# Kernel optimization log

Measured on AMD Instinct MI355X. Metric: run time of the kernel, lower is better.

The kernel has to match this reference:

```python
import jax, jax.numpy as jnp
import numpy as np

H = 2048      # hidden_size
L = 350       # max_length

def setup_inputs() -> dict:
    key = jax.random.key(0)
    ks = jax.random.split(key, 12)
    s = 0.02
    return {
        "input": jax.random.normal(ks[0], (1, 1, H), jnp.float32),
        "hidden": jax.random.normal(ks[1], (1, 1, H), jnp.float32),
        "encoder_outputs": jax.random.normal(ks[2], (L, H), jnp.float32),
        # nn.Linear(2H, L)
        "attn_W": jax.random.normal(ks[3], (L, 2 * H), jnp.float32) * s,
        "attn_b": jax.random.normal(ks[4], (L,), jnp.float32) * s,
        # nn.Linear(2H, H)
        "comb_W": jax.random.normal(ks[5], (H, 2 * H), jnp.float32) * s,
        "comb_b": jax.random.normal(ks[6], (H,), jnp.float32) * s,
        # nn.GRU(H, H) single layer weights (PyTorch layout: [3H, H])
        "w_ih": jax.random.normal(ks[7], (3 * H, H), jnp.float32) * s,
        "w_hh": jax.random.normal(ks[8], (3 * H, H), jnp.float32) * s,
        "b_ih": jax.random.normal(ks[9], (3 * H,), jnp.float32) * s,
        "b_hh": jax.random.normal(ks[10], (3 * H,), jnp.float32) * s,
    }

def reference(input, hidden, encoder_outputs, attn_W, attn_b, comb_W, comb_b, w_ih, w_hh, b_ih, b_hh):
    x = input.reshape(1, H)          # (1, H)  == reshape(input,(1,1,H))[0]
    h = hidden[0]                    # (1, H)
    # Bahdanau-style attention over fixed max_length slots
    attn_weights = jax.nn.softmax(jnp.concatenate([x, h], axis=1) @ attn_W.T + attn_b, axis=1)  # (1, L)
    context = attn_weights @ encoder_outputs                                                    # (1, H)
    # combine + relu (dropout is defined but never applied in the original forward)
    g = jax.nn.relu(jnp.concatenate([x, context], axis=1) @ comb_W.T + comb_b)                  # (1, H)
    # single GRU step (PyTorch gate order: reset, update, new)
    gi = g @ w_ih.T + b_ih           # (1, 3H)
    gh = h @ w_hh.T + b_hh           # (1, 3H)
    i_r, i_z, i_n = jnp.split(gi, 3, axis=1)
    h_r, h_z, h_n = jnp.split(gh, 3, axis=1)
    r = jax.nn.sigmoid(i_r + h_r)
    z = jax.nn.sigmoid(i_z + h_z)
    n = jnp.tanh(i_n + r * h_n)
    h_new = (1.0 - z) * n + z * h    # (1, H)
    output = h_new[None]             # (1, 1, H)
    return (output, h_new[None], attn_weights)
```

## Files before the change

### kernel.cpp

```cpp
#include <hip/hip_runtime.h>
#include <math.h>

#define H 2048
#define L 350
#define NB 1024
#define NREP 16
#define MAGIC 0x7FC0FFEEu
#define BOUND 65536

#define LOG_B0 0
#define CTX_B0 88
#define GHB_B0 152

#define OFF_GH   512
#define OFF_CTXR 8192
#define OFF_GR   40960
#define OFF_MK   73728

#define SLOTA 0
#define SLOTB (88*16)
#define SLOTC (SLOTB+64*16)
#define SLOTG (SLOTC+912*16)
#define SUPC  (SLOTG+1024*16)
#define SUPG  (SUPC+32*16)

#define VMCNT0() asm volatile("s_waitcnt vmcnt(0)" ::: "memory")

__device__ __forceinline__ float cload(const float* p) {
    return __hip_atomic_load(p, __ATOMIC_RELAXED, __HIP_MEMORY_SCOPE_AGENT);
}
__device__ __forceinline__ void cstore(float* p, float v) {
    __hip_atomic_store(p, v, __ATOMIC_RELAXED, __HIP_MEMORY_SCOPE_AGENT);
}
__device__ __forceinline__ unsigned long long cload64(const unsigned long long* p) {
    return __hip_atomic_load(p, __ATOMIC_RELAXED, __HIP_MEMORY_SCOPE_AGENT);
}
__device__ __forceinline__ void postmk(unsigned* p) {
    __hip_atomic_store(p, MAGIC, __ATOMIC_RELAXED, __HIP_MEMORY_SCOPE_SYSTEM);
}
__device__ __forceinline__ unsigned peekmk(const unsigned* p) {
    return __hip_atomic_load(p, __ATOMIC_RELAXED, __HIP_MEMORY_SCOPE_SYSTEM);
}
__device__ __forceinline__ void waitslots(const unsigned* base, int n) {
    const int t = threadIdx.x;
    for (int s = t; s < n; s += 256)
        for (int it = 0; it < BOUND; ++it) {
            if (peekmk(&base[s * 16]) == MAGIC) break;
            __builtin_amdgcn_s_sleep(8);
        }
    __syncthreads();
}

__device__ __forceinline__ float dot4(float4 a, float4 b, float acc) {
    acc = fmaf(a.x, b.x, acc);
    acc = fmaf(a.y, b.y, acc);
    acc = fmaf(a.z, b.z, acc);
    acc = fmaf(a.w, b.w, acc);
    return acc;
}
__device__ __forceinline__ float wsum(float v) {
    #pragma unroll
    for (int m = 1; m < 64; m <<= 1) v += __shfl_xor(v, m, 64);
    return v;
}
__device__ __forceinline__ float wmax(float v) {
    #pragma unroll
    for (int m = 1; m < 64; m <<= 1) v = fmaxf(v, __shfl_xor(v, m, 64));
    return v;
}

__device__ __forceinline__ void gh_row(int row, int lane,
    const float4* h4, const float* w_hh, const float* b_hh, float* gh)
{
    const float4* Wr = reinterpret_cast<const float4*>(w_hh + (size_t)row * H);
    float a0 = 0.f, a1 = 0.f, a2 = 0.f, a3 = 0.f;
    #pragma unroll
    for (int k = 0; k < 8; k += 4) {
        a0 = dot4(Wr[lane + (k + 0) * 64], h4[lane + (k + 0) * 64], a0);
        a1 = dot4(Wr[lane + (k + 1) * 64], h4[lane + (k + 1) * 64], a1);
        a2 = dot4(Wr[lane + (k + 2) * 64], h4[lane + (k + 2) * 64], a2);
        a3 = dot4(Wr[lane + (k + 3) * 64], h4[lane + (k + 3) * 64], a3);
    }
    const float acc = wsum((a0 + a1) + (a2 + a3));
    if (lane == 0) cstore(&gh[row], acc + b_hh[row]);
}

__global__ __launch_bounds__(256, 4) void fused_decoder(
    const float* __restrict__ input, const float* __restrict__ hidden,
    const float* __restrict__ enc,
    const float* __restrict__ attn_W, const float* __restrict__ attn_b,
    const float* __restrict__ comb_W, const float* __restrict__ comb_b,
    const float* __restrict__ w_ih, const float* __restrict__ w_hh,
    const float* __restrict__ b_ih, const float* __restrict__ b_hh,
    float* __restrict__ out, float* __restrict__ ws)
{
    __shared__ __align__(16) float sh[2048];
    __shared__ float smax[4], ssum[4];
    __shared__ float part[8][32];
    __shared__ float red[4];
    __shared__ float p3[4][3];

    float* logits = ws;
    float* gh     = ws + OFF_GH;
    float* ctxrep = ws + OFF_CTXR;
    float* grep   = ws + OFF_GR;
    unsigned* mk  = (unsigned*)(ws + OFF_MK);

    const int b = blockIdx.x, tid = threadIdx.x;
    const int wv = tid >> 6, lane = tid & 63;
    const float4* x4 = reinterpret_cast<const float4*>(input);
    const float4* h4 = reinterpret_cast<const float4*>(hidden);

    if (b < CTX_B0) {
        const int r = b * 4 + wv;
        if (r < L) {
            const float4* Wr = reinterpret_cast<const float4*>(attn_W + (size_t)r * (2 * H));
            float a0 = 0.f, a1 = 0.f, a2 = 0.f, a3 = 0.f;
            #pragma unroll
            for (int k = 0; k < 8; k += 4) {
                a0 = dot4(Wr[lane + (k+0)*64], x4[lane + (k+0)*64], a0);
                a1 = dot4(Wr[lane + (k+1)*64], x4[lane + (k+1)*64], a1);
                a2 = dot4(Wr[lane + (k+2)*64], x4[lane + (k+2)*64], a2);
                a3 = dot4(Wr[lane + (k+3)*64], x4[lane + (k+3)*64], a3);
            }
            #pragma unroll
            for (int k = 0; k < 8; k += 4) {
                a0 = dot4(Wr[512 + lane + (k+0)*64], h4[lane + (k+0)*64], a0);
                a1 = dot4(Wr[512 + lane + (k+1)*64], h4[lane + (k+1)*64], a1);
                a2 = dot4(Wr[512 + lane + (k+2)*64], h4[lane + (k+2)*64], a2);
                a3 = dot4(Wr[512 + lane + (k+3)*64], h4[lane + (k+3)*64], a3);
            }
            const float acc = wsum((a0 + a1) + (a2 + a3));
            if (lane == 0) cstore(&logits[r], acc + attn_b[r]);
        }
        VMCNT0();
        __syncthreads();
        if (tid == 0) postmk(&mk[SLOTA + b * 16]);
        if (b < 40) {
            if (wv == 0) gh_row(6104 + b, lane, h4, w_hh, b_hh, gh);
            VMCNT0();
            __syncthreads();
            if (tid == 0) postmk(&mk[SLOTC + (872 + b) * 16]);
        }
    } else if (b < GHB_B0) {
        const int cb = b - CTX_B0;
        waitslots(&mk[SLOTA], 88);
        float v0 = (tid < L) ? cload(&logits[tid]) : -INFINITY;
        float v1 = (tid + 256 < L) ? cload(&logits[tid + 256]) : -INFINITY;
        float m = wmax(fmaxf(v0, v1));
        if (lane == 0) smax[wv] = m;
        __syncthreads();
        m = fmaxf(fmaxf(smax[0], smax[1]), fmaxf(smax[2], smax[3]));
        float e0 = (tid < L) ? expf(v0 - m) : 0.f;
        float e1 = (tid + 256 < L) ? expf(v1 - m) : 0.f;
        float s = wsum(e0 + e1);
        if (lane == 0) ssum[wv] = s;
        __syncthreads();
        const float inv = 1.f / (ssum[0] + ssum[1] + ssum[2] + ssum[3]);
        if (tid < L) sh[tid] = e0 * inv;
        if (tid + 256 < L) sh[tid + 256] = e1 * inv;
        if (cb == 0) {
            if (tid < L) out[2 * H + tid] = e0 * inv;
            if (tid + 256 < L) out[2 * H + tid + 256] = e1 * inv;
        }
        __syncthreads();
        const int col_l = tid & 31, k = tid >> 5;
        const float* ec = enc + cb * 32 + col_l;
        float a0 = 0.f, a1 = 0.f, a2 = 0.f, a3 = 0.f;
        int j = k;
        for (; j + 24 < L; j += 32) {
            a0 = fmaf(sh[j],      ec[(size_t)j * H],        a0);
            a1 = fmaf(sh[j + 8],  ec[(size_t)(j + 8) * H],  a1);
            a2 = fmaf(sh[j + 16], ec[(size_t)(j + 16) * H], a2);
            a3 = fmaf(sh[j + 24], ec[(size_t)(j + 24) * H], a3);
        }
        for (; j < L; j += 8) a0 = fmaf(sh[j], ec[(size_t)j * H], a0);
        part[k][col_l] = (a0 + a1) + (a2 + a3);
        __syncthreads();
        if (tid < 32) {
            const float acc = part[0][tid] + part[1][tid] + part[2][tid] + part[3][tid]
                            + part[4][tid] + part[5][tid] + part[6][tid] + part[7][tid];
            #pragma unroll
            for (int rp = 0; rp < NREP; ++rp)
                cstore(&ctxrep[rp * 2048 + cb * 32 + tid], acc);
        }
        VMCNT0();
        __syncthreads();
        if (tid == 0) postmk(&mk[SLOTB + cb * 16]);
    } else {
        const int m = b - GHB_B0;
        #pragma unroll
        for (int j = 0; j < 7; ++j)
            if ((j & 3) == wv) gh_row(m * 7 + j, lane, h4, w_hh, b_hh, gh);
        VMCNT0();
        __syncthreads();
        if (tid == 0) postmk(&mk[SLOTC + m * 16]);
    }

    waitslots(&mk[SLOTB], 64);
    {
        unsigned long long* sh64 = reinterpret_cast<unsigned long long*>(sh);
        const unsigned long long* c64 =
            reinterpret_cast<const unsigned long long*>(ctxrep + (b & (NREP - 1)) * 2048);
        for (int i = tid; i < H / 2; i += 256) sh64[i] = cload64(&c64[i]);
    }
    __syncthreads();
    {
        const float4* c4 = reinterpret_cast<const float4*>(sh);
        #pragma unroll
        for (int rr = 0; rr < 2; ++rr) {
            const int r = b * 2 + rr;
            const float4* Wr = reinterpret_cast<const float4*>(comb_W + (size_t)r * (2 * H));
            float a0 = dot4(Wr[tid],       x4[tid],       0.f);
            float a1 = dot4(Wr[tid + 256], x4[tid + 256], 0.f);
            float a2 = dot4(Wr[tid + 512], c4[tid],       0.f);
            float a3 = dot4(Wr[tid + 768], c4[tid + 256], 0.f);
            const float acc = wsum((a0 + a1) + (a2 + a3));
            if (lane == 0) red[wv] = acc;
            __syncthreads();
            if (tid == 0) {
                const float gval = fmaxf(red[0] + red[1] + red[2] + red[3] + comb_b[r], 0.f);
                #pragma unroll
                for (int rp = 0; rp < NREP; ++rp) cstore(&grep[rp * 2048 + r], gval);
            }
            __syncthreads();
        }
    }
    VMCNT0();
    if (tid == 0) postmk(&mk[SLOTG + b * 16]);

    if (b >= 88 && b < 120) {
        const int w = b - 88;
        const int cfrom = w * 29, cto = (cfrom + 29 < 912) ? cfrom + 29 : 912;
        if (tid < cto - cfrom) {
            for (int it = 0; it < BOUND; ++it) {
                if (peekmk(&mk[SLOTC + (cfrom + tid) * 16]) == MAGIC) break;
                __builtin_amdgcn_s_sleep(8);
            }
        } else if (tid >= 64 && tid < 96) {
            for (int it = 0; it < BOUND; ++it) {
                if (peekmk(&mk[SLOTG + (w * 32 + tid - 64) * 16]) == MAGIC) break;
                __builtin_amdgcn_s_sleep(8);
            }
        }
        __syncthreads();
        if (tid == 0) { postmk(&mk[SUPC + w * 16]); postmk(&mk[SUPG + w * 16]); }
    }

    {
        const int t = tid;
        if (t < 32) {
            for (int it = 0; it < BOUND; ++it) {
                if (peekmk(&mk[SUPC + t * 16]) == MAGIC) break;
                __builtin_amdgcn_s_sleep(8);
            }
        } else if (t >= 64 && t < 96) {
            for (int it = 0; it < BOUND; ++it) {
                if (peekmk(&mk[SUPG + (t - 64) * 16]) == MAGIC) break;
                __builtin_amdgcn_s_sleep(8);
            }
        }
        __syncthreads();
    }
    {
        unsigned long long* sh64 = reinterpret_cast<unsigned long long*>(sh);
        const unsigned long long* g64 =
            reinterpret_cast<const unsigned long long*>(grep + (b & (NREP - 1)) * 2048);
        for (int i = tid; i < H / 2; i += 256) sh64[i] = cload64(&g64[i]);
    }
    __syncthreads();
    {
        const float4* g4 = reinterpret_cast<const float4*>(sh);
        #pragma unroll
        for (int cc = 0; cc < 2; ++cc) {
            const int col = b * 2 + cc;
            const float4* W0 = reinterpret_cast<const float4*>(w_ih + (size_t)col * H);
            const float4* W1 = reinterpret_cast<const float4*>(w_ih + (size_t)(col + H) * H);
            const float4* W2 = reinterpret_cast<const float4*>(w_ih + (size_t)(col + 2 * H) * H);
            const float4 gv0 = g4[tid], gv1 = g4[tid + 256];
            float ar = dot4(W0[tid], gv0, 0.f); ar = dot4(W0[tid + 256], gv1, ar);
            float az = dot4(W1[tid], gv0, 0.f); az = dot4(W1[tid + 256], gv1, az);
            float an = dot4(W2[tid], gv0, 0.f); an = dot4(W2[tid + 256], gv1, an);
            ar = wsum(ar); az = wsum(az); an = wsum(an);
            if (lane == 0) { p3[wv][0] = ar; p3[wv][1] = az; p3[wv][2] = an; }
            __syncthreads();
            if (tid == 0) {
                const float ir  = p3[0][0] + p3[1][0] + p3[2][0] + p3[3][0] + b_ih[col];
                const float iz  = p3[0][1] + p3[1][1] + p3[2][1] + p3[3][1] + b_ih[col + H];
                const float in_ = p3[0][2] + p3[1][2] + p3[2][2] + p3[3][2] + b_ih[col + 2 * H];
                const float r = 1.f / (1.f + expf(-(ir + cload(&gh[col]))));
                const float z = 1.f / (1.f + expf(-(iz + cload(&gh[col + H]))));
                const float n = tanhf(in_ + r * cload(&gh[col + 2 * H]));
                const float hnew = (1.f - z) * n + z * hidden[col];
                out[col] = hnew;
                out[H + col] = hnew;
            }
            __syncthreads();
        }
    }
}

extern "C" void kernel_launch(void* const* d_in, const int* in_sizes, int n_in,
                              void* d_out, int out_size, void* d_ws, size_t ws_size,
                              hipStream_t stream)
{
    const float* input  = (const float*)d_in[0];
    const float* hidden = (const float*)d_in[1];
    const float* enc    = (const float*)d_in[2];
    const float* attn_W = (const float*)d_in[3];
    const float* attn_b = (const float*)d_in[4];
    const float* comb_W = (const float*)d_in[5];
    const float* comb_b = (const float*)d_in[6];
    const float* w_ih   = (const float*)d_in[7];
    const float* w_hh   = (const float*)d_in[8];
    const float* b_ih   = (const float*)d_in[9];
    const float* b_hh   = (const float*)d_in[10];
    float* out = (float*)d_out;
    float* ws  = (float*)d_ws;

    fused_decoder<<<NB, 256, 0, stream>>>(
        input, hidden, enc, attn_W, attn_b, comb_W, comb_b,
        w_ih, w_hh, b_ih, b_hh, out, ws);
}
```

Before: 32.17 us.

## Double block size to 512 threads and split rows across two thread teams

Blocks grow from 256 to 512 threads. Per-block work that used to run as two sequential iterations (two comb rows, two GRU columns) now runs as two 256-thread teams in parallel, which removes a loop and its barriers. The w_hh rows are rebalanced so the attention blocks' spare waves compute gh tail rows alongside the logits, and the gh blocks take 7 or 6 rows each. The aim is shorter per-block critical paths across the grid-wide flag chain. The risk is lower occupancy per CU with the larger blocks under launch_bounds(512,8), and every block must still be co-resident for the spin-wait barriers to work.

```diff
diff --git a/kernel.cpp b/kernel.cpp
--- a/kernel.cpp
+++ b/kernel.cpp
@@ -8,9 +8,9 @@
 #define MAGIC 0x7FC0FFEEu
 #define BOUND 65536
 
-#define LOG_B0 0
 #define CTX_B0 88
 #define GHB_B0 152
+#define GH_TAIL 5792
 
 #define OFF_GH   512
 #define OFF_CTXR 8192
@@ -20,7 +20,7 @@
 #define SLOTA 0
 #define SLOTB (88*16)
 #define SLOTC (SLOTB+64*16)
-#define SLOTG (SLOTC+912*16)
+#define SLOTG (SLOTC+960*16)
 #define SUPC  (SLOTG+1024*16)
 #define SUPG  (SUPC+32*16)
 
@@ -41,13 +41,14 @@
 __device__ __forceinline__ unsigned peekmk(const unsigned* p) {
     return __hip_atomic_load(p, __ATOMIC_RELAXED, __HIP_MEMORY_SCOPE_SYSTEM);
 }
+__device__ __forceinline__ void pollone(const unsigned* p) {
+    for (int it = 0; it < BOUND; ++it) {
+        if (peekmk(p) == MAGIC) break;
+        __builtin_amdgcn_s_sleep(8);
+    }
+}
 __device__ __forceinline__ void waitslots(const unsigned* base, int n) {
-    const int t = threadIdx.x;
-    for (int s = t; s < n; s += 256)
-        for (int it = 0; it < BOUND; ++it) {
-            if (peekmk(&base[s * 16]) == MAGIC) break;
-            __builtin_amdgcn_s_sleep(8);
-        }
+    for (int s = threadIdx.x; s < n; s += 512) pollone(&base[s * 16]);
     __syncthreads();
 }
 
@@ -85,7 +86,7 @@
     if (lane == 0) cstore(&gh[row], acc + b_hh[row]);
 }
 
-__global__ __launch_bounds__(256, 4) void fused_decoder(
+__global__ __launch_bounds__(512, 8) void fused_decoder(
     const float* __restrict__ input, const float* __restrict__ hidden,
     const float* __restrict__ enc,
     const float* __restrict__ attn_W, const float* __restrict__ attn_b,
@@ -95,10 +96,10 @@
     float* __restrict__ out, float* __restrict__ ws)
 {
     __shared__ __align__(16) float sh[2048];
-    __shared__ float smax[4], ssum[4];
-    __shared__ float part[8][32];
-    __shared__ float red[4];
-    __shared__ float p3[4][3];
+    __shared__ float smax[8], ssum[8];
+    __shared__ float part[16][32];
+    __shared__ float red[2][4];
+    __shared__ float p3[2][4][3];
 
     float* logits = ws;
     float* gh     = ws + OFF_GH;
@@ -112,74 +113,67 @@
     const float4* h4 = reinterpret_cast<const float4*>(hidden);
 
     if (b < CTX_B0) {
-        const int r = b * 4 + wv;
-        if (r < L) {
-            const float4* Wr = reinterpret_cast<const float4*>(attn_W + (size_t)r * (2 * H));
-            float a0 = 0.f, a1 = 0.f, a2 = 0.f, a3 = 0.f;
-            #pragma unroll
-            for (int k = 0; k < 8; k += 4) {
-                a0 = dot4(Wr[lane + (k+0)*64], x4[lane + (k+0)*64], a0);
-                a1 = dot4(Wr[lane + (k+1)*64], x4[lane + (k+1)*64], a1);
-                a2 = dot4(Wr[lane + (k+2)*64], x4[lane + (k+2)*64], a2);
-                a3 = dot4(Wr[lane + (k+3)*64], x4[lane + (k+3)*64], a3);
+        if (wv < 4) {
+            const int r = b * 4 + wv;
+            if (r < L) {
+                const float4* Wr = reinterpret_cast<const float4*>(attn_W + (size_t)r * (2 * H));
+                float a0 = 0.f, a1 = 0.f, a2 = 0.f, a3 = 0.f;
+                #pragma unroll
+                for (int k = 0; k < 8; k += 4) {
+                    a0 = dot4(Wr[lane + (k+0)*64], x4[lane + (k+0)*64], a0);
+                    a1 = dot4(Wr[lane + (k+1)*64], x4[lane + (k+1)*64], a1);
+                    a2 = dot4(Wr[lane + (k+2)*64], x4[lane + (k+2)*64], a2);
+                    a3 = dot4(Wr[lane + (k+3)*64], x4[lane + (k+3)*64], a3);
+                }
+                #pragma unroll
+                for (int k = 0; k < 8; k += 4) {
+                    a0 = dot4(Wr[512 + lane + (k+0)*64], h4[lane + (k+0)*64], a0);
+                    a1 = dot4(Wr[512 + lane + (k+1)*64], h4[lane + (k+1)*64], a1);
+                    a2 = dot4(Wr[512 + lane + (k+2)*64], h4[lane + (k+2)*64], a2);
+                    a3 = dot4(Wr[512 + lane + (k+3)*64], h4[lane + (k+3)*64], a3);
+                }
+                const float acc = wsum((a0 + a1) + (a2 + a3));
+                if (lane == 0) cstore(&logits[r], acc + attn_b[r]);
             }
-            #pragma unroll
-            for (int k = 0; k < 8; k += 4) {
-                a0 = dot4(Wr[512 + lane + (k+0)*64], h4[lane + (k+0)*64], a0);
-                a1 = dot4(Wr[512 + lane + (k+1)*64], h4[lane + (k+1)*64], a1);
-                a2 = dot4(Wr[512 + lane + (k+2)*64], h4[lane + (k+2)*64], a2);
-                a3 = dot4(Wr[512 + lane + (k+3)*64], h4[lane + (k+3)*64], a3);
-            }
-            const float acc = wsum((a0 + a1) + (a2 + a3));
-            if (lane == 0) cstore(&logits[r], acc + attn_b[r]);
+        } else {
+            gh_row(GH_TAIL + b * 4 + (wv - 4), lane, h4, w_hh, b_hh, gh);
         }
         VMCNT0();
         __syncthreads();
-        if (tid == 0) postmk(&mk[SLOTA + b * 16]);
-        if (b < 40) {
-            if (wv == 0) gh_row(6104 + b, lane, h4, w_hh, b_hh, gh);
-            VMCNT0();
-            __syncthreads();
-            if (tid == 0) postmk(&mk[SLOTC + (872 + b) * 16]);
-        }
+        if (tid == 0) { postmk(&mk[SLOTA + b * 16]); postmk(&mk[SLOTC + (872 + b) * 16]); }
     } else if (b < GHB_B0) {
         const int cb = b - CTX_B0;
         waitslots(&mk[SLOTA], 88);
         float v0 = (tid < L) ? cload(&logits[tid]) : -INFINITY;
-        float v1 = (tid + 256 < L) ? cload(&logits[tid + 256]) : -INFINITY;
-        float m = wmax(fmaxf(v0, v1));
+        float m = wmax(v0);
         if (lane == 0) smax[wv] = m;
         __syncthreads();
-        m = fmaxf(fmaxf(smax[0], smax[1]), fmaxf(smax[2], smax[3]));
+        m = fmaxf(fmaxf(fmaxf(smax[0], smax[1]), fmaxf(smax[2], smax[3])),
+                  fmaxf(fmaxf(smax[4], smax[5]), fmaxf(smax[6], smax[7])));
         float e0 = (tid < L) ? expf(v0 - m) : 0.f;
-        float e1 = (tid + 256 < L) ? expf(v1 - m) : 0.f;
-        float s = wsum(e0 + e1);
+        float s = wsum(e0);
         if (lane == 0) ssum[wv] = s;
         __syncthreads();
-        const float inv = 1.f / (ssum[0] + ssum[1] + ssum[2] + ssum[3]);
+        const float inv = 1.f / (((ssum[0] + ssum[1]) + (ssum[2] + ssum[3]))
+                               + ((ssum[4] + ssum[5]) + (ssum[6] + ssum[7])));
         if (tid < L) sh[tid] = e0 * inv;
-        if (tid + 256 < L) sh[tid + 256] = e1 * inv;
-        if (cb == 0) {
-            if (tid < L) out[2 * H + tid] = e0 * inv;
-            if (tid + 256 < L) out[2 * H + tid + 256] = e1 * inv;
-        }
+        if (cb == 0 && tid < L) out[2 * H + tid] = e0 * inv;
         __syncthreads();
         const int col_l = tid & 31, k = tid >> 5;
         const float* ec = enc + cb * 32 + col_l;
-        float a0 = 0.f, a1 = 0.f, a2 = 0.f, a3 = 0.f;
+        float a0 = 0.f, a1 = 0.f;
         int j = k;
-        for (; j + 24 < L; j += 32) {
+        for (; j + 16 < L; j += 32) {
             a0 = fmaf(sh[j],      ec[(size_t)j * H],        a0);
-            a1 = fmaf(sh[j + 8],  ec[(size_t)(j + 8) * H],  a1);
-            a2 = fmaf(sh[j + 16], ec[(size_t)(j + 16) * H], a2);
-            a3 = fmaf(sh[j + 24], ec[(size_t)(j + 24) * H], a3);
-        }
-        for (; j < L; j += 8) a0 = fmaf(sh[j], ec[(size_t)j * H], a0);
-        part[k][col_l] = (a0 + a1) + (a2 + a3);
+            a1 = fmaf(sh[j + 16], ec[(size_t)(j + 16) * H], a1);
+        }
+        for (; j < L; j += 16) a0 = fmaf(sh[j], ec[(size_t)j * H], a0);
+        part[k][col_l] = a0 + a1;
         __syncthreads();
         if (tid < 32) {
-            const float acc = part[0][tid] + part[1][tid] + part[2][tid] + part[3][tid]
-                            + part[4][tid] + part[5][tid] + part[6][tid] + part[7][tid];
+            float acc = 0.f;
+            #pragma unroll
+            for (int kk = 0; kk < 16; ++kk) acc += part[kk][tid];
             #pragma unroll
             for (int rp = 0; rp < NREP; ++rp)
                 cstore(&ctxrep[rp * 2048 + cb * 32 + tid], acc);
@@ -189,9 +183,9 @@
         if (tid == 0) postmk(&mk[SLOTB + cb * 16]);
     } else {
         const int m = b - GHB_B0;
-        #pragma unroll
-        for (int j = 0; j < 7; ++j)
-            if ((j & 3) == wv) gh_row(m * 7 + j, lane, h4, w_hh, b_hh, gh);
+        const int start = (m < 560) ? m * 7 : 3920 + (m - 560) * 6;
+        const int count = (m < 560) ? 7 : 6;
+        if (wv < count) gh_row(start + wv, lane, h4, w_hh, b_hh, gh);
         VMCNT0();
         __syncthreads();
         if (tid == 0) postmk(&mk[SLOTC + m * 16]);
@@ -202,100 +196,74 @@
         unsigned long long* sh64 = reinterpret_cast<unsigned long long*>(sh);
         const unsigned long long* c64 =
             reinterpret_cast<const unsigned long long*>(ctxrep + (b & (NREP - 1)) * 2048);
-        for (int i = tid; i < H / 2; i += 256) sh64[i] = cload64(&c64[i]);
-    }
-    __syncthreads();
-    {
+        for (int i = tid; i < H / 2; i += 512) sh64[i] = cload64(&c64[i]);
+    }
+    __syncthreads();
+    {
+        const int team = tid >> 8, ttid = tid & 255, twv = (tid >> 6) & 3;
         const float4* c4 = reinterpret_cast<const float4*>(sh);
-        #pragma unroll
-        for (int rr = 0; rr < 2; ++rr) {
-            const int r = b * 2 + rr;
-            const float4* Wr = reinterpret_cast<const float4*>(comb_W + (size_t)r * (2 * H));
-            float a0 = dot4(Wr[tid],       x4[tid],       0.f);
-            float a1 = dot4(Wr[tid + 256], x4[tid + 256], 0.f);
-            float a2 = dot4(Wr[tid + 512], c4[tid],       0.f);
-            float a3 = dot4(Wr[tid + 768], c4[tid + 256], 0.f);
-            const float acc = wsum((a0 + a1) + (a2 + a3));
-            if (lane == 0) red[wv] = acc;
-            __syncthreads();
-            if (tid == 0) {
-                const float gval = fmaxf(red[0] + red[1] + red[2] + red[3] + comb_b[r], 0.f);
-                #pragma unroll
-                for (int rp = 0; rp < NREP; ++rp) cstore(&grep[rp * 2048 + r], gval);
-            }
-            __syncthreads();
-        }
+        const int r = b * 2 + team;
+        const float4* Wr = reinterpret_cast<const float4*>(comb_W + (size_t)r * (2 * H));
+        float a0 = dot4(Wr[ttid],       x4[ttid],       0.f);
+        float a1 = dot4(Wr[ttid + 256], x4[ttid + 256], 0.f);
+        float a2 = dot4(Wr[ttid + 512], c4[ttid],       0.f);
+        float a3 = dot4(Wr[ttid + 768], c4[ttid + 256], 0.f);
+        const float acc = wsum((a0 + a1) + (a2 + a3));
+        if (lane == 0) red[team][twv] = acc;
+        __syncthreads();
+        if (ttid == 0) {
+            const float gval = fmaxf(red[team][0] + red[team][1] + red[team][2]
+                                     + red[team][3] + comb_b[r], 0.f);
+            #pragma unroll
+            for (int rp = 0; rp < NREP; ++rp) cstore(&grep[rp * 2048 + r], gval);
+        }
+        __syncthreads();
     }
     VMCNT0();
     if (tid == 0) postmk(&mk[SLOTG + b * 16]);
 
-    if (b >= 88 && b < 120) {
-        const int w = b - 88;
-        const int cfrom = w * 29, cto = (cfrom + 29 < 912) ? cfrom + 29 : 912;
-        if (tid < cto - cfrom) {
-            for (int it = 0; it < BOUND; ++it) {
-                if (peekmk(&mk[SLOTC + (cfrom + tid) * 16]) == MAGIC) break;
-                __builtin_amdgcn_s_sleep(8);
-            }
-        } else if (tid >= 64 && tid < 96) {
-            for (int it = 0; it < BOUND; ++it) {
-                if (peekmk(&mk[SLOTG + (w * 32 + tid - 64) * 16]) == MAGIC) break;
-                __builtin_amdgcn_s_sleep(8);
-            }
-        }
+    if (b >= CTX_B0 && b < CTX_B0 + 32) {
+        const int w = b - CTX_B0;
+        if (tid < 30) pollone(&mk[SLOTC + (w * 30 + tid) * 16]);
+        else if (tid >= 64 && tid < 96) pollone(&mk[SLOTG + (w * 32 + tid - 64) * 16]);
         __syncthreads();
         if (tid == 0) { postmk(&mk[SUPC + w * 16]); postmk(&mk[SUPG + w * 16]); }
     }
 
-    {
-        const int t = tid;
-        if (t < 32) {
-            for (int it = 0; it < BOUND; ++it) {
-                if (peekmk(&mk[SUPC + t * 16]) == MAGIC) break;
-                __builtin_amdgcn_s_sleep(8);
-            }
-        } else if (t >= 64 && t < 96) {
-            for (int it = 0; it < BOUND; ++it) {
-                if (peekmk(&mk[SUPG + (t - 64) * 16]) == MAGIC) break;
-                __builtin_amdgcn_s_sleep(8);
-            }
-        }
-        __syncthreads();
-    }
+    if (tid < 32) pollone(&mk[SUPC + tid * 16]);
+    else if (tid >= 64 && tid < 96) pollone(&mk[SUPG + (tid - 64) * 16]);
+    __syncthreads();
     {
         unsigned long long* sh64 = reinterpret_cast<unsigned long long*>(sh);
         const unsigned long long* g64 =
             reinterpret_cast<const unsigned long long*>(grep + (b & (NREP - 1)) * 2048);
-        for (int i = tid; i < H / 2; i += 256) sh64[i] = cload64(&g64[i]);
-    }
-    __syncthreads();
-    {
+        for (int i = tid; i < H / 2; i += 512) sh64[i] = cload64(&g64[i]);
+    }
+    __syncthreads();
+    {
+        const int team = tid >> 8, ttid = tid & 255, twv = (tid >> 6) & 3;
         const float4* g4 = reinterpret_cast<const float4*>(sh);
-        #pragma unroll
-        for (int cc = 0; cc < 2; ++cc) {
-            const int col = b * 2 + cc;
-            const float4* W0 = reinterpret_cast<const float4*>(w_ih + (size_t)col * H);
-            const float4* W1 = reinterpret_cast<const float4*>(w_ih + (size_t)(col + H) * H);
-            const float4* W2 = reinterpret_cast<const float4*>(w_ih + (size_t)(col + 2 * H) * H);
-            const float4 gv0 = g4[tid], gv1 = g4[tid + 256];
-            float ar = dot4(W0[tid], gv0, 0.f); ar = dot4(W0[tid + 256], gv1, ar);
-            float az = dot4(W1[tid], gv0, 0.f); az = dot4(W1[tid + 256], gv1, az);
-            float an = dot4(W2[tid], gv0, 0.f); an = dot4(W2[tid + 256], gv1, an);
-            ar = wsum(ar); az = wsum(az); an = wsum(an);
-            if (lane == 0) { p3[wv][0] = ar; p3[wv][1] = az; p3[wv][2] = an; }
-            __syncthreads();
-            if (tid == 0) {
-                const float ir  = p3[0][0] + p3[1][0] + p3[2][0] + p3[3][0] + b_ih[col];
-                const float iz  = p3[0][1] + p3[1][1] + p3[2][1] + p3[3][1] + b_ih[col + H];
-                const float in_ = p3[0][2] + p3[1][2] + p3[2][2] + p3[3][2] + b_ih[col + 2 * H];
-                const float r = 1.f / (1.f + expf(-(ir + cload(&gh[col]))));
-                const float z = 1.f / (1.f + expf(-(iz + cload(&gh[col + H]))));
-                const float n = tanhf(in_ + r * cload(&gh[col + 2 * H]));
-                const float hnew = (1.f - z) * n + z * hidden[col];
-                out[col] = hnew;
-                out[H + col] = hnew;
-            }
-            __syncthreads();
+        const int col = b * 2 + team;
+        const float4* W0 = reinterpret_cast<const float4*>(w_ih + (size_t)col * H);
+        const float4* W1 = reinterpret_cast<const float4*>(w_ih + (size_t)(col + H) * H);
+        const float4* W2 = reinterpret_cast<const float4*>(w_ih + (size_t)(col + 2 * H) * H);
+        const float4 gv0 = g4[ttid], gv1 = g4[ttid + 256];
+        float ar = dot4(W0[ttid], gv0, 0.f); ar = dot4(W0[ttid + 256], gv1, ar);
+        float az = dot4(W1[ttid], gv0, 0.f); az = dot4(W1[ttid + 256], gv1, az);
+        float an = dot4(W2[ttid], gv0, 0.f); an = dot4(W2[ttid + 256], gv1, an);
+        ar = wsum(ar); az = wsum(az); an = wsum(an);
+        if (lane == 0) { p3[team][twv][0] = ar; p3[team][twv][1] = az; p3[team][twv][2] = an; }
+        __syncthreads();
+        if (ttid == 0) {
+            const float ir  = p3[team][0][0] + p3[team][1][0] + p3[team][2][0] + p3[team][3][0] + b_ih[col];
+            const float iz  = p3[team][0][1] + p3[team][1][1] + p3[team][2][1] + p3[team][3][1] + b_ih[col + H];
+            const float in_ = p3[team][0][2] + p3[team][1][2] + p3[team][2][2] + p3[team][3][2] + b_ih[col + 2 * H];
+            const float r = 1.f / (1.f + expf(-(ir + cload(&gh[col]))));
+            const float z = 1.f / (1.f + expf(-(iz + cload(&gh[col + H]))));
+            const float n = tanhf(in_ + r * cload(&gh[col + 2 * H]));
+            const float hnew = (1.f - z) * n + z * hidden[col];
+            out[col] = hnew;
+            out[H + col] = hnew;
         }
     }
 }
@@ -318,7 +286,7 @@
     float* out = (float*)d_out;
     float* ws  = (float*)d_ws;
 
-    fused_decoder<<<NB, 256, 0, stream>>>(
+    fused_decoder<<<NB, 512, 0, stream>>>(
         input, hidden, enc, attn_W, attn_b, comb_W, comb_b,
         w_ih, w_hh, b_ih, b_hh, out, ws);
 }
```

Result: slower. 34.19 us (+6.3%).
